# Performance work log

Measured on AMD Instinct MI355X. Metric: run time of the kernel, lower is better.

## Reference

```python
import jax, jax.numpy as jnp
import numpy as np

B, T = 1, 1024
HID = 2048
H, HKV, D = 16, 4, 128
G = H // HKV          # kv groups
TOPK = 256
HI, DI = 4, 32        # indexer heads / head dim


def _rotate_half(x):
    x1, x2 = jnp.split(x, 2, axis=-1)
    return jnp.concatenate([-x2, x1], axis=-1)


def _apply_rotary(x, cos, sin):
    # x: (B,T,H,D), cos/sin: (1,T,1,D)
    return x * cos + _rotate_half(x) * sin


def _rms_norm(x):
    eps = jnp.finfo(x.dtype).eps
    return x * jax.lax.rsqrt(jnp.mean(x * x, axis=-1, keepdims=True) + eps)


def setup_inputs() -> dict:
    key = jax.random.key(0)
    ks = jax.random.split(key, 9)
    s = 0.02
    x = jax.random.normal(ks[0], (B, T, HID), jnp.float32)
    # rotary tables
    inv_freq = 1.0 / (10000.0 ** (jnp.arange(0, D, 2, dtype=jnp.float32) / D))
    freqs = jnp.outer(jnp.arange(T, dtype=jnp.float32), inv_freq)   # (T, D/2)
    emb = jnp.concatenate([freqs, freqs], axis=-1)                  # (T, D)
    cos = jnp.cos(emb)[None, :, None, :]
    sin = jnp.sin(emb)[None, :, None, :]
    Wq = jax.random.normal(ks[1], (HID, H * D), jnp.float32) * s
    Wk = jax.random.normal(ks[2], (HID, HKV * D), jnp.float32) * s
    Wv = jax.random.normal(ks[3], (HID, HKV * D), jnp.float32) * s
    Wo = jax.random.normal(ks[4], (H * D, HID), jnp.float32) * s
    Wqi = jax.random.normal(ks[5], (HID, HI * DI), jnp.float32) * s
    Wwi = jax.random.normal(ks[6], (HID, HI), jnp.float32) * s
    Wki = jax.random.normal(ks[7], (HID, DI), jnp.float32) * s
    return {"x": x, "cos": cos, "sin": sin, "Wq": Wq, "Wk": Wk, "Wv": Wv,
            "Wo": Wo, "Wqi": Wqi, "Wwi": Wwi, "Wki": Wki}


def reference(x, cos, sin, Wq, Wk, Wv, Wo, Wqi, Wwi, Wki):
    b, t, _ = x.shape
    q = (x @ Wq).reshape(b, t, H, D)
    k = (x @ Wk).reshape(b, t, HKV, D)
    v = (x @ Wv).reshape(b, t, HKV, D)
    q = _rms_norm(_apply_rotary(q, cos, sin))
    k = _rms_norm(_apply_rotary(k, cos, sin))

    # ---- lightning indexer: I[t,s] = sum_j w[t,j] * relu(q_i[t,j] . k_i[s]) ----
    qi = (x @ Wqi).reshape(b, t, HI, DI)
    wi = x @ Wwi                                   # (B,T,HI)
    ki = x @ Wki                                   # (B,T,DI)
    raw = jax.nn.relu(jnp.einsum('bthd,bsd->bths', qi, ki))
    idx_scores = jnp.einsum('bths,bth->bts', raw, wi)     # (B,T,T)

    pos = jnp.arange(t)
    causal = pos[None, :] <= pos[:, None]                 # (T,T) valid s<=t
    masked = jnp.where(causal[None], idx_scores, -jnp.inf)
    _, top_idx = jax.lax.top_k(masked, TOPK)              # (B,T,K) int32

    # gather selected K/V: (B,T,K,HKV,D)
    gather = jax.vmap(lambda arr, idx: arr[idx])          # per-batch fancy gather
    sel_k = gather(k, top_idx)
    sel_v = gather(v, top_idx)
    sel_mask = top_idx <= pos[None, :, None]              # (B,T,K)

    # grouped-query attention over selected tokens (avoid repeat_interleave)
    q5 = q.reshape(b, t, HKV, G, D)                       # q head h -> kv head h//G
    scale = D ** -0.5
    scores = jnp.einsum('btngd,btknd->btngk', q5, sel_k) * scale
    scores = jnp.where(sel_mask[:, :, None, None, :], scores, -jnp.inf)
    probs = jax.nn.softmax(scores, axis=-1)
    attn = jnp.einsum('btngk,btknd->btngd', probs, sel_v)  # (B,T,HKV,G,D)
    out = attn.reshape(b, t, H * D) @ Wo
    return out
```

## Files before the change

### kernel.cpp

```cpp
#include <hip/hip_runtime.h>
#include <hip/hip_bf16.h>
#include <math.h>

#define T_    1024
#define HID_  2048
#define NH    16
#define NKV   4
#define DH    128
#define TOPK_ 256
#define HI_   4
#define DI_   32
#define NPROJ 3072
#define NIDX  164
#define KSPLIT 8
#define KCHUNK 256

#ifndef INFINITY
#define INFINITY (__builtin_inff())
#endif

typedef __attribute__((ext_vector_type(8))) short bf16x8;
typedef __attribute__((ext_vector_type(4))) float f32x4;

__device__ inline unsigned int packbf(float f) {
    unsigned int u = __float_as_uint(f);
    return (u + 0x7fffu + ((u >> 16) & 1u)) >> 16;
}

#define GLDS16(g, l) __builtin_amdgcn_global_load_lds( \
    (const __attribute__((address_space(1))) void*)(g), \
    (__attribute__((address_space(3))) void*)(l), 16, 0, 0)

__device__ inline void tcast_body(const float* __restrict__ W, unsigned short* __restrict__ Wt,
                                  int N, int bx, int by, int tid, float (*tile)[33]) {
    const int n0 = bx * 32, k0 = by * 32;
    const int tx = tid & 31, ty = tid >> 5;
#pragma unroll
    for (int i = 0; i < 4; ++i)
        tile[ty + i * 8][tx] = W[(size_t)(k0 + ty + i * 8) * N + (n0 + tx)];
    __syncthreads();
#pragma unroll
    for (int i = 0; i < 4; ++i) {
        int n = n0 + ty + i * 8;
        Wt[(size_t)n * HID_ + k0 + tx] = (unsigned short)packbf(tile[tx][ty + i * 8]);
    }
}

__device__ inline void gemm64_body(const unsigned short* __restrict__ A,
                                   const unsigned short* __restrict__ Bt,
                                   float* __restrict__ C, int K, int ldc,
                                   int bx, int by, int tid,
                                   unsigned short* As, unsigned short* Bs) {
    const int lane = tid & 63, w = tid >> 6;
    const int wr = w >> 1, wc = w & 1;
    const int brow = by * 64, bcol = bx * 64;
    const int l15 = lane & 15, lq = lane >> 4;

    f32x4 acc[2][2] = {};

    const int srow = tid >> 3;
    const int gsrc = ((tid & 7) ^ (srow & 7)) * 8;
    const unsigned short* ga  = A  + (size_t)(brow + srow) * K + gsrc;
    const unsigned short* ga2 = ga + (size_t)32 * K;
    const unsigned short* gb  = Bt + (size_t)(bcol + srow) * K + gsrc;
    const unsigned short* gb2 = gb + (size_t)32 * K;
    unsigned short* la  = &As[(size_t)tid * 8];
    unsigned short* la2 = &As[(size_t)(tid + 256) * 8];
    unsigned short* lb  = &Bs[(size_t)tid * 8];
    unsigned short* lb2 = &Bs[(size_t)(tid + 256) * 8];

    for (int k0 = 0; k0 < K; k0 += 64) {
        GLDS16(ga + k0,  la);
        GLDS16(ga2 + k0, la2);
        GLDS16(gb + k0,  lb);
        GLDS16(gb2 + k0, lb2);
        __syncthreads();
        bf16x8 fa[2][2], fb[2][2];
#pragma unroll
        for (int m = 0; m < 2; ++m)
#pragma unroll
            for (int kk = 0; kk < 2; ++kk) {
                int row = wr * 32 + m * 16 + l15;
                fa[m][kk] = *(const bf16x8*)&As[row * 64 + (((kk * 4 + lq) ^ (l15 & 7)) * 8)];
            }
#pragma unroll
        for (int nn = 0; nn < 2; ++nn)
#pragma unroll
            for (int kk = 0; kk < 2; ++kk) {
                int row = wc * 32 + nn * 16 + l15;
                fb[nn][kk] = *(const bf16x8*)&Bs[row * 64 + (((kk * 4 + lq) ^ (l15 & 7)) * 8)];
            }
#pragma unroll
        for (int kk = 0; kk < 2; ++kk)
#pragma unroll
            for (int m = 0; m < 2; ++m)
#pragma unroll
                for (int nn = 0; nn < 2; ++nn)
                    acc[m][nn] = __builtin_amdgcn_mfma_f32_16x16x32_bf16(fa[m][kk], fb[nn][kk], acc[m][nn], 0, 0, 0);
        __syncthreads();
    }
#pragma unroll
    for (int m = 0; m < 2; ++m)
#pragma unroll
        for (int nn = 0; nn < 2; ++nn)
#pragma unroll
            for (int q = 0; q < 4; ++q) {
                int row = brow + wr * 32 + m * 16 + lq * 4 + q;
                int col = bcol + wc * 32 + nn * 16 + l15;
                C[(size_t)row * ldc + col] = acc[m][nn][q];
            }
}

__global__ __launch_bounds__(256) void prep1(const float* __restrict__ x,
                                             const float* __restrict__ Wq,
                                             const float* __restrict__ Wk,
                                             const float* __restrict__ Wv,
                                             const float* __restrict__ Wqi,
                                             const float* __restrict__ Wwi,
                                             const float* __restrict__ Wki,
                                             unsigned short* __restrict__ xb,
                                             unsigned short* __restrict__ WtAll,
                                             float* __restrict__ Wi) {
    __shared__ float tile[32][33];
    int bid = blockIdx.x;
    const int tid = threadIdx.x;
    if (bid < 4096) { tcast_body(Wq, WtAll, HID_, bid & 63, bid >> 6, tid, tile); return; }
    bid -= 4096;
    if (bid < 1024) { tcast_body(Wk, WtAll + (size_t)2048 * HID_, 512, bid & 15, bid >> 4, tid, tile); return; }
    bid -= 1024;
    if (bid < 1024) { tcast_body(Wv, WtAll + (size_t)2560 * HID_, 512, bid & 15, bid >> 4, tid, tile); return; }
    bid -= 1024;
    if (bid < 1024) {
        int e = bid * 256 + tid;
        const float4* p = (const float4*)(x + (size_t)e * 8);
        float4 a = p[0], b = p[1];
        uint4 r;
        r.x = packbf(a.x) | (packbf(a.y) << 16);
        r.y = packbf(a.z) | (packbf(a.w) << 16);
        r.z = packbf(b.x) | (packbf(b.y) << 16);
        r.w = packbf(b.z) | (packbf(b.w) << 16);
        *(uint4*)(xb + (size_t)e * 8) = r;
        return;
    }
    bid -= 1024;
    {
        int e = bid * 256 + tid;
        if (e >= HID_ * NIDX) return;
        int k = e / NIDX, c = e - k * NIDX;
        float v;
        if (c < 128) v = Wqi[(size_t)k * 128 + c];
        else if (c < 132) v = Wwi[(size_t)k * 4 + (c - 128)];
        else v = Wki[(size_t)k * 32 + (c - 132)];
        Wi[e] = v;
    }
}

__global__ __launch_bounds__(256) void fusedA(const unsigned short* __restrict__ xb,
                                              const unsigned short* __restrict__ WtAll,
                                              float* __restrict__ proj,
                                              const float* __restrict__ x,
                                              const float* __restrict__ Wi,
                                              float* __restrict__ Cpart) {
    __shared__ __align__(16) char smem[64 * 64 * 2 * 2];
    const int tid = threadIdx.x;
    int bid = blockIdx.x;

    if (bid < 768) {
        unsigned short* As = (unsigned short*)smem;
        unsigned short* Bs = As + 64 * 64;
        gemm64_body(xb, WtAll, proj, HID_, NPROJ, bid % 48, bid / 48, tid, As, Bs);
        return;
    }
    float (*As2)[68] = (float(*)[68])smem;
    float (*Bs2)[68] = As2 + 16;
    int s = bid - 768;
    const int bx = s % 3, by = (s / 3) % 16, z = s / 48;
    const int tx = tid & 15, ty = tid >> 4;
    const int brow = by * 64, bcol = bx * 64;
    const int kbeg = z * KCHUNK, kend = kbeg + KCHUNK;
    const int M = T_, N = NIDX, K = HID_;

    const int ar = tid >> 2, ac4 = (tid & 3) * 4;
    const int br = tid >> 4, bc4 = (tid & 15) * 4;

    float acc[4][4];
#pragma unroll
    for (int i = 0; i < 4; ++i)
#pragma unroll
        for (int j = 0; j < 4; ++j) acc[i][j] = 0.f;

    for (int k0 = kbeg; k0 < kend; k0 += 16) {
        float4 va = *(const float4*)&x[(size_t)(brow + ar) * K + k0 + ac4];
        float4 vb;
        int col = bcol + bc4;
        if (col <= N - 4) vb = *(const float4*)&Wi[(size_t)(k0 + br) * N + col];
        else vb = (float4){0.f, 0.f, 0.f, 0.f};
        As2[ac4 + 0][ar] = va.x;
        As2[ac4 + 1][ar] = va.y;
        As2[ac4 + 2][ar] = va.z;
        As2[ac4 + 3][ar] = va.w;
        *(float4*)&Bs2[br][bc4] = vb;
        __syncthreads();
#pragma unroll
        for (int kk = 0; kk < 16; ++kk) {
            float4 a4 = *(const float4*)&As2[kk][ty * 4];
            float4 b4 = *(const float4*)&Bs2[kk][tx * 4];
            float a[4] = {a4.x, a4.y, a4.z, a4.w};
            float b[4] = {b4.x, b4.y, b4.z, b4.w};
#pragma unroll
            for (int i = 0; i < 4; ++i)
#pragma unroll
                for (int j = 0; j < 4; ++j) acc[i][j] += a[i] * b[j];
        }
        __syncthreads();
    }
#pragma unroll
    for (int i = 0; i < 4; ++i) {
        int r = brow + ty * 4 + i;
#pragma unroll
        for (int j = 0; j < 4; ++j) {
            int c = bcol + tx * 4 + j;
            if (c < N) Cpart[((size_t)z * M + r) * N + c] = acc[i][j];
        }
    }
}

__global__ __launch_bounds__(256) void reduce_k(const float* __restrict__ Cpart,
                                                float* __restrict__ Cout,
                                                float* __restrict__ kib, int MN) {
    int e = blockIdx.x * 256 + threadIdx.x;
    if (e >= MN) return;
    float s = 0.f;
#pragma unroll
    for (int z = 0; z < KSPLIT; ++z) s += Cpart[(size_t)z * MN + e];
    Cout[e] = s;
    int t = e / NIDX, c = e - t * NIDX;
    if (c >= 132) kib[(size_t)t * DI_ + (c - 132)] = s;
}

__global__ __launch_bounds__(256) void fusedB(const float* __restrict__ proj,
                                              const float* __restrict__ cosb,
                                              const float* __restrict__ sinb,
                                              unsigned short* __restrict__ qbb,
                                              unsigned short* __restrict__ kbb,
                                              unsigned int* __restrict__ vbb,
                                              const float* __restrict__ Wo,
                                              unsigned short* __restrict__ Wot,
                                              const float* __restrict__ proji,
                                              const float* __restrict__ kib,
                                              int* __restrict__ idxout) {
    __shared__ float tile[32][33];
    const int tid = threadIdx.x;
    int bid = blockIdx.x;

    if (bid < 5376) {
        const int w = tid >> 6, lane = tid & 63;
        const int u = bid * 4 + w;
        const int t = u / 21, h = u - t * 21;
        if (h < 20) {
            const float* row;
            unsigned short* dst;
            if (h < 16) { row = proj + (size_t)t * NPROJ + h * DH;               dst = qbb + ((size_t)t * NH + h) * DH; }
            else        { row = proj + (size_t)t * NPROJ + HID_ + (h - 16) * DH; dst = kbb + ((size_t)t * NKV + (h - 16)) * DH; }
            float a = row[lane], b = row[lane + 64];
            float c0 = cosb[t * DH + lane],      s0 = sinb[t * DH + lane];
            float c1 = cosb[t * DH + lane + 64], s1 = sinb[t * DH + lane + 64];
            float r0 = a * c0 - b * s0;
            float r1 = b * c1 + a * s1;
            float ss = r0 * r0 + r1 * r1;
#pragma unroll
            for (int o = 32; o > 0; o >>= 1) ss += __shfl_xor(ss, o);
            float inv = rsqrtf(ss * (1.0f / 128.0f) + 1.1920929e-07f);
            dst[lane]      = (unsigned short)packbf(r0 * inv);
            dst[lane + 64] = (unsigned short)packbf(r1 * inv);
        } else {
            const float* src = proj + (size_t)t * NPROJ + HID_ + 512;
#pragma unroll
            for (int i = 0; i < 4; ++i) {
                int c2 = lane + i * 64;
                vbb[(size_t)t * 256 + c2] = packbf(src[2 * c2]) | (packbf(src[2 * c2 + 1]) << 16);
            }
        }
        return;
    }
    bid -= 5376;
    if (bid < 4096) {
        tcast_body(Wo, Wot, HID_, bid & 63, bid >> 6, tid, tile);
        return;
    }
    bid -= 4096;
    {
        const int t = bid;
        int* orow = idxout + (size_t)t * TOPK_;
        if (t < TOPK_) { orow[tid] = tid; return; }

        __shared__ float qsh[128];
        __shared__ float wsh[4];
        if (tid < 128) qsh[tid] = proji[(size_t)t * NIDX + tid];
        else if (tid < 132) wsh[tid - 128] = proji[(size_t)t * NIDX + tid];
        __syncthreads();

        const int n = t + 1;
        const int lane = tid & 63, wave = tid >> 6;

        unsigned int key[4];
#pragma unroll
        for (int j = 0; j < 4; ++j) {
            int s = j * 256 + tid;
            if (s < n) {
                const float4* kr = (const float4*)&kib[(size_t)s * DI_];
                float4 k4[8];
#pragma unroll
                for (int d4 = 0; d4 < 8; ++d4) k4[d4] = kr[d4];
                float sc = 0.f;
#pragma unroll
                for (int h = 0; h < HI_; ++h) {
                    float d = 0.f;
#pragma unroll
                    for (int d4 = 0; d4 < 8; ++d4) {
                        const float* qp = &qsh[h * 32 + d4 * 4];
                        d += k4[d4].x * qp[0] + k4[d4].y * qp[1] +
                             k4[d4].z * qp[2] + k4[d4].w * qp[3];
                    }
                    sc += wsh[h] * fmaxf(d, 0.f);
                }
                unsigned int u = __float_as_uint(sc);
                key[j] = (u & 0x80000000u) ? ~u : (u | 0x80000000u);
            } else key[j] = 0u;
        }

        __shared__ int wcnt[2][4];
        unsigned int prefix = 0;
#pragma unroll 1
        for (int b = 31; b >= 0; --b) {
            unsigned int cand = prefix | (1u << b);
            int c = (key[0] >= cand) + (key[1] >= cand) + (key[2] >= cand) + (key[3] >= cand);
#pragma unroll
            for (int o = 32; o > 0; o >>= 1) c += __shfl_xor(c, o);
            if (lane == 0) wcnt[b & 1][wave] = c;
            __syncthreads();
            int total = wcnt[b & 1][0] + wcnt[b & 1][1] + wcnt[b & 1][2] + wcnt[b & 1][3];
            if (total >= TOPK_) prefix = cand;
        }
        const unsigned int T = prefix;

        __shared__ int posc;
        __shared__ int eqtot[4][4];
        __syncthreads();
        {
            int c = (key[0] > T) + (key[1] > T) + (key[2] > T) + (key[3] > T);
#pragma unroll
            for (int o = 32; o > 0; o >>= 1) c += __shfl_xor(c, o);
            if (lane == 0) wcnt[0][wave] = c;
        }
        if (tid == 0) posc = 0;

        int e[4]; int myp[4];
#pragma unroll
        for (int j = 0; j < 4; ++j) {
            e[j] = (key[j] == T) ? 1 : 0;
            unsigned long long m = __ballot(e[j]);
            myp[j] = __popcll(m & ((1ull << lane) - 1ull));
            if (lane == 0) eqtot[j][wave] = __popcll(m);
        }
        __syncthreads();
        const int cntGT = wcnt[0][0] + wcnt[0][1] + wcnt[0][2] + wcnt[0][3];
        const int need = TOPK_ - cntGT;

#pragma unroll
        for (int j = 0; j < 4; ++j)
            if (key[j] > T) {
                int p = atomicAdd(&posc, 1);
                orow[p] = j * 256 + tid;
            }
        int runbase = 0;
#pragma unroll
        for (int j = 0; j < 4; ++j) {
            int wavebase = 0;
#pragma unroll
            for (int w2 = 0; w2 < 4; ++w2) if (w2 < wave) wavebase += eqtot[j][w2];
            int g = runbase + wavebase + myp[j];
            if (e[j] && g < need) orow[cntGT + g] = j * 256 + tid;
            runbase += eqtot[j][0] + eqtot[j][1] + eqtot[j][2] + eqtot[j][3];
        }
    }
}

__global__ __launch_bounds__(256) void gemm64(const unsigned short* __restrict__ A,
                                              const unsigned short* __restrict__ Bt,
                                              float* __restrict__ C,
                                              int K, int ldc) {
    __shared__ unsigned short As[64 * 64];
    __shared__ unsigned short Bs[64 * 64];
    gemm64_body(A, Bt, C, K, ldc, blockIdx.x, blockIdx.y, threadIdx.x, As, Bs);
}

__global__ __launch_bounds__(256) void attn7(const unsigned short* __restrict__ qbb,
                                             const unsigned short* __restrict__ kbb,
                                             const unsigned short* __restrict__ vbb,
                                             const int* __restrict__ idx,
                                             unsigned short* __restrict__ attnb) {
    const int t = blockIdx.x, n = blockIdx.y;
    const int tid = threadIdx.x, lane = tid & 63, w = tid >> 6;
    const int C = (t + 1 < TOPK_) ? t + 1 : TOPK_;
    const int l15 = lane & 15, lq = lane >> 4;

    __shared__ int sidx[TOPK_];
    __shared__ float sp[4][TOPK_];
    __shared__ float sinv[4];
    __shared__ unsigned short P[4][264];
    __shared__ unsigned short Vs[2][32 * 128];

    sidx[tid] = idx[(size_t)t * TOPK_ + tid];
    __syncthreads();

#define STAGE_V(buf, tau)                                                          \
    {                                                                              \
        _Pragma("unroll")                                                          \
        for (int it = 0; it < 2; ++it) {                                           \
            int c = tid + it * 256;                                                \
            int r = c >> 4, doff = (c & 15) * 8;                                   \
            int gs = doff ^ (((r >> 3) & 3) << 4);                                 \
            GLDS16(&vbb[((size_t)sidx[(tau) * 32 + r] * NKV + n) * DH + gs],       \
                   &Vs[buf][(size_t)c * 8]);                                       \
        }                                                                          \
    }

    STAGE_V(0, 0);

    const size_t qrow = (size_t)t * NH + n * 4 + (l15 < 4 ? l15 : 3);
    bf16x8 qf[4];
#pragma unroll
    for (int ks = 0; ks < 4; ++ks)
        qf[ks] = *(const bf16x8*)&qbb[qrow * DH + ks * 32 + lq * 8];

#pragma unroll
    for (int tt = 0; tt < 4; ++tt) {
        const int tile = w * 4 + tt;
        const int tok = tile * 16 + l15;
        const unsigned short* krow = &kbb[((size_t)sidx[tok] * NKV + n) * DH];
        f32x4 acc = {0.f, 0.f, 0.f, 0.f};
        __builtin_amdgcn_s_setprio(1);
#pragma unroll
        for (int ks = 0; ks < 4; ++ks) {
            bf16x8 yf = *(const bf16x8*)&krow[ks * 32 + lq * 8];
            acc = __builtin_amdgcn_mfma_f32_16x16x32_bf16(qf[ks], yf, acc, 0, 0, 0);
        }
        __builtin_amdgcn_s_setprio(0);
        if (lane < 16) {
            int j = tile * 16 + lane;
            bool ok = j < C;
#pragma unroll
            for (int q = 0; q < 4; ++q)
                sp[q][j] = ok ? acc[q] * 0.08838834764831845f : -INFINITY;
        }
    }
    __syncthreads();

    {
        float v0 = sp[w][lane], v1 = sp[w][lane + 64],
              v2 = sp[w][lane + 128], v3 = sp[w][lane + 192];
        float m = fmaxf(fmaxf(v0, v1), fmaxf(v2, v3));
#pragma unroll
        for (int o = 32; o > 0; o >>= 1) m = fmaxf(m, __shfl_xor(m, o));
        float e0 = expf(v0 - m), e1 = expf(v1 - m), e2 = expf(v2 - m), e3 = expf(v3 - m);
        float sum = e0 + e1 + e2 + e3;
#pragma unroll
        for (int o = 32; o > 0; o >>= 1) sum += __shfl_xor(sum, o);
        if (lane == 0) sinv[w] = 1.f / sum;
        P[w][lane]       = (unsigned short)packbf(e0);
        P[w][lane + 64]  = (unsigned short)packbf(e1);
        P[w][lane + 128] = (unsigned short)packbf(e2);
        P[w][lane + 192] = (unsigned short)packbf(e3);
    }
    __syncthreads();

    const int prow = (l15 < 4) ? l15 : 3;
    f32x4 pacc[2] = {};
#pragma unroll
    for (int tau = 0; tau < 8; ++tau) {
        const unsigned short* Vb = Vs[tau & 1];
        if (tau < 7) STAGE_V((tau + 1) & 1, tau + 1);
        bf16x8 xf = *(const bf16x8*)&P[prow][tau * 32 + lq * 8];
        const int colr0 = ((2 * w + 0) * 16 + l15) ^ (lq << 4);
        const int colr1 = ((2 * w + 1) * 16 + l15) ^ (lq << 4);
        bf16x8 yf0, yf1;
#pragma unroll
        for (int j = 0; j < 8; ++j) {
            yf0[j] = (short)Vb[(lq * 8 + j) * 128 + colr0];
            yf1[j] = (short)Vb[(lq * 8 + j) * 128 + colr1];
        }
        __builtin_amdgcn_s_setprio(1);
        pacc[0] = __builtin_amdgcn_mfma_f32_16x16x32_bf16(xf, yf0, pacc[0], 0, 0, 0);
        pacc[1] = __builtin_amdgcn_mfma_f32_16x16x32_bf16(xf, yf1, pacc[1], 0, 0, 0);
        __builtin_amdgcn_s_setprio(0);
        __syncthreads();
    }
#undef STAGE_V

    if (lane < 16) {
#pragma unroll
        for (int dt = 0; dt < 2; ++dt)
#pragma unroll
            for (int q = 0; q < 4; ++q)
                attnb[(size_t)(t * NH + n * 4 + q) * DH + (2 * w + dt) * 16 + l15] =
                    (unsigned short)packbf(pacc[dt][q] * sinv[q]);
    }
}

extern "C" void kernel_launch(void* const* d_in, const int* in_sizes, int n_in,
                              void* d_out, int out_size, void* d_ws, size_t ws_size,
                              hipStream_t stream) {
    const float* x    = (const float*)d_in[0];
    const float* cosb = (const float*)d_in[1];
    const float* sinb = (const float*)d_in[2];
    const float* Wq   = (const float*)d_in[3];
    const float* Wk   = (const float*)d_in[4];
    const float* Wv   = (const float*)d_in[5];
    const float* Wo   = (const float*)d_in[6];
    const float* Wqi  = (const float*)d_in[7];
    const float* Wwi  = (const float*)d_in[8];
    const float* Wki  = (const float*)d_in[9];
    float* out = (float*)d_out;

    unsigned short* xb    = (unsigned short*)d_ws;
    unsigned short* WtAll = xb + 2097152;
    float*  proj  = (float*)(WtAll + 6291456);
    float*  Wi    = proj + 3145728;
    float*  proji = Wi + 335872;
    float*  kib   = proji + 167936;
    int*    idxb  = (int*)(kib + 1048576);
    unsigned short* kbb   = (unsigned short*)(idxb + 262144);
    unsigned short* vbb   = kbb + 524288;
    unsigned short* attnb = vbb + 524288;
    unsigned short* Wot   = WtAll;
    unsigned short* qbb   = xb;
    float* Cpart = (float*)kbb;

    prep1<<<dim3(8480), dim3(256), 0, stream>>>(x, Wq, Wk, Wv, Wqi, Wwi, Wki, xb, WtAll, Wi);

    fusedA<<<dim3(1152), dim3(256), 0, stream>>>(xb, WtAll, proj, x, Wi, Cpart);

    reduce_k<<<dim3((T_ * NIDX + 255) / 256), dim3(256), 0, stream>>>(Cpart, proji, kib, T_ * NIDX);

    fusedB<<<dim3(10496), dim3(256), 0, stream>>>(proj, cosb, sinb, qbb, kbb, (unsigned int*)vbb,
                                                  Wo, Wot, proji, kib, idxb);

    attn7<<<dim3(T_, NKV), dim3(256), 0, stream>>>(qbb, kbb, vbb, idxb, attnb);

    gemm64<<<dim3(HID_ / 64, T_ / 64), dim3(256), 0, stream>>>(attnb, Wot, out, HID_, HID_);
}
```

Before: 170.7 us.

## Double-buffer LDS tiles in the bf16 MFMA GEMM to overlap loads with compute

Gives the shared 64x64 GEMM body two LDS stages. The global-to-LDS loads for the next K tile are issued before the MFMAs on the current tile, so each iteration only needs the existing trailing barrier instead of a load-then-barrier step. The aim is to hide global memory latency in the projection GEMM and the output GEMM. In exchange, LDS per block doubles to 32 KB in both fusedA and gemm64, which may reduce how many blocks fit on a CU.

```diff
diff --git a/kernel.cpp b/kernel.cpp
--- a/kernel.cpp
+++ b/kernel.cpp
@@ -64,31 +64,41 @@
     const unsigned short* ga2 = ga + (size_t)32 * K;
     const unsigned short* gb  = Bt + (size_t)(bcol + srow) * K + gsrc;
     const unsigned short* gb2 = gb + (size_t)32 * K;
-    unsigned short* la  = &As[(size_t)tid * 8];
-    unsigned short* la2 = &As[(size_t)(tid + 256) * 8];
-    unsigned short* lb  = &Bs[(size_t)tid * 8];
-    unsigned short* lb2 = &Bs[(size_t)(tid + 256) * 8];
-
-    for (int k0 = 0; k0 < K; k0 += 64) {
-        GLDS16(ga + k0,  la);
-        GLDS16(ga2 + k0, la2);
-        GLDS16(gb + k0,  lb);
-        GLDS16(gb2 + k0, lb2);
-        __syncthreads();
+    const int lo1 = tid * 8, lo2 = (tid + 256) * 8;
+
+    GLDS16(ga,  &As[lo1]);
+    GLDS16(ga2, &As[lo2]);
+    GLDS16(gb,  &Bs[lo1]);
+    GLDS16(gb2, &Bs[lo2]);
+    __syncthreads();
+
+    const int NT = K >> 6;
+    for (int kt = 0; kt < NT; ++kt) {
+        const int cur = (kt & 1) * 4096;
+        if (kt + 1 < NT) {
+            const int nxt = ((kt + 1) & 1) * 4096;
+            const int k0 = (kt + 1) << 6;
+            GLDS16(ga + k0,  &As[nxt + lo1]);
+            GLDS16(ga2 + k0, &As[nxt + lo2]);
+            GLDS16(gb + k0,  &Bs[nxt + lo1]);
+            GLDS16(gb2 + k0, &Bs[nxt + lo2]);
+        }
+        const unsigned short* Ac = &As[cur];
+        const unsigned short* Bc = &Bs[cur];
         bf16x8 fa[2][2], fb[2][2];
 #pragma unroll
         for (int m = 0; m < 2; ++m)
 #pragma unroll
             for (int kk = 0; kk < 2; ++kk) {
                 int row = wr * 32 + m * 16 + l15;
-                fa[m][kk] = *(const bf16x8*)&As[row * 64 + (((kk * 4 + lq) ^ (l15 & 7)) * 8)];
+                fa[m][kk] = *(const bf16x8*)&Ac[row * 64 + (((kk * 4 + lq) ^ (l15 & 7)) * 8)];
             }
 #pragma unroll
         for (int nn = 0; nn < 2; ++nn)
 #pragma unroll
             for (int kk = 0; kk < 2; ++kk) {
                 int row = wc * 32 + nn * 16 + l15;
-                fb[nn][kk] = *(const bf16x8*)&Bs[row * 64 + (((kk * 4 + lq) ^ (l15 & 7)) * 8)];
+                fb[nn][kk] = *(const bf16x8*)&Bc[row * 64 + (((kk * 4 + lq) ^ (l15 & 7)) * 8)];
             }
 #pragma unroll
         for (int kk = 0; kk < 2; ++kk)
@@ -161,13 +171,13 @@
                                               const float* __restrict__ x,
                                               const float* __restrict__ Wi,
                                               float* __restrict__ Cpart) {
-    __shared__ __align__(16) char smem[64 * 64 * 2 * 2];
+    __shared__ __align__(16) char smem[64 * 64 * 2 * 2 * 2];
     const int tid = threadIdx.x;
     int bid = blockIdx.x;
 
     if (bid < 768) {
         unsigned short* As = (unsigned short*)smem;
-        unsigned short* Bs = As + 64 * 64;
+        unsigned short* Bs = As + 8192;
         gemm64_body(xb, WtAll, proj, HID_, NPROJ, bid % 48, bid / 48, tid, As, Bs);
         return;
     }
@@ -390,8 +400,8 @@
                                               const unsigned short* __restrict__ Bt,
                                               float* __restrict__ C,
                                               int K, int ldc) {
-    __shared__ unsigned short As[64 * 64];
-    __shared__ unsigned short Bs[64 * 64];
+    __shared__ unsigned short As[2 * 64 * 64];
+    __shared__ unsigned short Bs[2 * 64 * 64];
     gemm64_body(A, Bt, C, K, ldc, blockIdx.x, blockIdx.y, threadIdx.x, As, Bs);
 }
 
```

Result: no change. 169.4 us (-0.7%).
